# Performance work log

Measured on AMD Instinct MI355X. Metric: run time of the kernel, lower is better.

## Reference

```python
import jax, jax.numpy as jnp
import numpy as np

N_NODES = 100000
N_EDGES = 1600000
D = 64


def setup_inputs() -> dict:
    key = jax.random.key(0)
    ks = jax.random.split(key, 7)
    x = jax.random.normal(ks[0], (N_NODES, D), dtype=jnp.float32)
    row = jax.random.randint(ks[1], (N_EDGES,), 0, N_NODES, dtype=jnp.int64)
    col = jax.random.randint(ks[2], (N_EDGES,), 0, N_NODES, dtype=jnp.int64)
    batch = jnp.zeros((N_NODES,), dtype=jnp.int64)
    # positive normalizer (e.g. degree-based); keep away from zero
    adj_norm = jax.random.uniform(ks[3], (N_NODES, 1), dtype=jnp.float32, minval=0.5, maxval=1.5)
    root_W = jax.random.normal(ks[4], (D, D), dtype=jnp.float32) / jnp.sqrt(D)
    root_b = jax.random.normal(ks[5], (D,), dtype=jnp.float32) * 0.01
    rel_W = jax.random.normal(ks[6], (D, D), dtype=jnp.float32) / jnp.sqrt(D)
    return {"x": x, "row": row, "col": col, "batch": batch, "adj_norm": adj_norm,
            "root_W": root_W, "root_b": root_b, "rel_W": rel_W}


def reference(x, row, col, batch, adj_norm, root_W, root_b, rel_W):
    # gather source features per edge, scatter-sum into destination nodes
    agg = jax.ops.segment_sum(x[row], col, num_segments=x.shape[0])  # [N, D]
    agg = agg / adj_norm
    rel = agg @ rel_W.T                      # Linear(bias=False)
    root = x @ root_W.T + root_b             # Linear(bias=True)
    return jax.nn.relu(rel + root)
```

## Files before the change

### kernel.cpp

```cpp
#include <hip/hip_runtime.h>

#define N_NODES 100000
#define N_EDGES 1600000
#define D 64
#define ROWW 128
#define NPB 128
#define NBUCK ((N_NODES + NPB - 1) / NPB)
#define CHUNK 8192
#define NCHUNK ((N_EDGES + CHUNK - 1) / CHUNK)
#define APAD 136

typedef __attribute__((ext_vector_type(8))) short bf16x8;
typedef __attribute__((ext_vector_type(4))) float f32x4;

__device__ __forceinline__ unsigned short f2bf(float f) {
    unsigned bits = __float_as_uint(f);
    bits += 0x7FFF + ((bits >> 16) & 1);
    return (unsigned short)(bits >> 16);
}

__global__ __launch_bounds__(256) void stage_x(const float* __restrict__ x,
                                               unsigned short* __restrict__ ab, int n8) {
    int t = blockIdx.x * 256 + threadIdx.x;
    if (t >= n8) return;
    int nrow = t >> 3, g = t & 7;
    const float4* xf = (const float4*)(x + (size_t)nrow * D + g * 8);
    float4 a = xf[0], b = xf[1];
    unsigned short u[8];
    u[0] = f2bf(a.x); u[1] = f2bf(a.y); u[2] = f2bf(a.z); u[3] = f2bf(a.w);
    u[4] = f2bf(b.x); u[5] = f2bf(b.y); u[6] = f2bf(b.z); u[7] = f2bf(b.w);
    *reinterpret_cast<uint4*>(ab + (size_t)nrow * ROWW + 64 + g * 8) =
        *reinterpret_cast<const uint4*>(u);
}

__global__ __launch_bounds__(256) void stage_w(const float* __restrict__ rel_W,
                                               const float* __restrict__ root_W,
                                               unsigned short* __restrict__ Wb) {
    int t = blockIdx.x * 256 + threadIdx.x;
    if (t >= 1024) return;
    int j = t >> 4, g = t & 15;
    const float* src = (g < 8) ? (rel_W + j * 64 + g * 8) : (root_W + j * 64 + (g - 8) * 8);
    unsigned short u[8];
    #pragma unroll
    for (int i = 0; i < 8; ++i) u[i] = f2bf(src[i]);
    *reinterpret_cast<uint4*>(Wb + j * ROWW + g * 8) = *reinterpret_cast<const uint4*>(u);
}

__global__ __launch_bounds__(1024) void hist_kernel(const int* __restrict__ col,
                                                    int* __restrict__ bucketTotals) {
    __shared__ int h[NBUCK];
    for (int k = threadIdx.x; k < NBUCK; k += 1024) h[k] = 0;
    __syncthreads();
    int base = blockIdx.x * CHUNK;
    #pragma unroll
    for (int it = 0; it < CHUNK / 1024; ++it) {
        int e = base + it * 1024 + threadIdx.x;
        if (e < N_EDGES) atomicAdd(&h[col[e] >> 7], 1);
    }
    __syncthreads();
    for (int k = threadIdx.x; k < NBUCK; k += 1024)
        if (h[k]) atomicAdd(&bucketTotals[k], h[k]);
}

__global__ __launch_bounds__(1024) void scan_kernel(const int* __restrict__ totals,
                                                    int* __restrict__ base_,
                                                    int* __restrict__ cursor) {
    int tid = threadIdx.x;
    int v = (tid < NBUCK) ? totals[tid] : 0;
    int lane = tid & 63, wave = tid >> 6;
    int s = v;
    #pragma unroll
    for (int o = 1; o < 64; o <<= 1) {
        int t = __shfl_up(s, o, 64);
        if (lane >= o) s += t;
    }
    __shared__ int ws[16];
    if (lane == 63) ws[wave] = s;
    __syncthreads();
    if (wave == 0 && lane < 16) {
        int w = ws[lane];
        #pragma unroll
        for (int o = 1; o < 16; o <<= 1) {
            int t = __shfl_up(w, o, 64);
            if (lane >= o) w += t;
        }
        ws[lane] = w;
    }
    __syncthreads();
    int excl = s - v + (wave ? ws[wave - 1] : 0);
    if (tid < NBUCK) { base_[tid] = excl; cursor[tid] = excl; }
}

__global__ __launch_bounds__(1024) void partition_kernel(const int* __restrict__ row,
                                                         const int* __restrict__ col,
                                                         int* __restrict__ cursor,
                                                         int* __restrict__ edges) {
    __shared__ int cnt[NBUCK];
    __shared__ int runStart[NBUCK];
    __shared__ int rank[NBUCK];
    for (int k = threadIdx.x; k < NBUCK; k += 1024) { cnt[k] = 0; rank[k] = 0; }
    __syncthreads();
    int base = blockIdx.x * CHUNK;
    #pragma unroll
    for (int it = 0; it < CHUNK / 1024; ++it) {
        int e = base + it * 1024 + threadIdx.x;
        if (e < N_EDGES) atomicAdd(&cnt[col[e] >> 7], 1);
    }
    __syncthreads();
    for (int k = threadIdx.x; k < NBUCK; k += 1024) {
        int c = cnt[k];
        runStart[k] = c ? atomicAdd(&cursor[k], c) : 0;
    }
    __syncthreads();
    #pragma unroll
    for (int it = 0; it < CHUNK / 1024; ++it) {
        int e = base + it * 1024 + threadIdx.x;
        if (e < N_EDGES) {
            int d = col[e];
            int b = d >> 7;
            int r = atomicAdd(&rank[b], 1);
            edges[runStart[b] + r] = ((d & (NPB - 1)) << 17) | row[e];
        }
    }
}

__global__ __launch_bounds__(512) void sort_kernel(const int* __restrict__ edges,
                                                   const int* __restrict__ base_,
                                                   const int* __restrict__ totals,
                                                   int* __restrict__ edge_src,
                                                   int* __restrict__ off,
                                                   int* __restrict__ deg) {
    __shared__ int cnt[NPB];
    __shared__ int offL[NPB];
    __shared__ int cur[NPB];
    int tid = threadIdx.x;
    int b = blockIdx.x;
    int base = base_[b];
    int tot = totals[b];

    if (tid < NPB) cnt[tid] = 0;
    __syncthreads();
    for (int i = base + tid; i < base + tot; i += 512)
        atomicAdd(&cnt[edges[i] >> 17], 1);
    __syncthreads();

    if (tid < 64) {
        int v0 = cnt[2 * tid], v1 = cnt[2 * tid + 1];
        int s = v0 + v1;
        #pragma unroll
        for (int o = 1; o < 64; o <<= 1) {
            int t = __shfl_up(s, o, 64);
            if (tid >= o) s += t;
        }
        offL[2 * tid]     = s - v1 - v0;
        offL[2 * tid + 1] = s - v1;
        cur[2 * tid]      = s - v1 - v0;
        cur[2 * tid + 1]  = s - v1;
    }
    __syncthreads();

    for (int i = base + tid; i < base + tot; i += 512) {
        int p = edges[i];
        int l = p >> 17;
        int r = atomicAdd(&cur[l], 1);
        edge_src[base + r] = p & 0x1FFFF;
    }

    if (tid < NPB) {
        int gn = b * NPB + tid;
        if (gn < N_NODES) {
            off[gn] = base + offL[tid];
            deg[gn] = cnt[tid];
        }
    }
}

__global__ __launch_bounds__(256) void agg_kernel(unsigned short* __restrict__ ab,
                                                  const int* __restrict__ edge_src,
                                                  const int* __restrict__ off,
                                                  const int* __restrict__ deg,
                                                  const float* __restrict__ adj_norm) {
    int w = (blockIdx.x * 256 + threadIdx.x) >> 6;
    if (w >= N_NODES) return;
    int lane = threadIdx.x & 63;
    int q = lane >> 4, sub = lane & 15;
    int s = off[w], dg = deg[w];
    const unsigned short* __restrict__ xh = ab + 64 + sub * 4;

    float a0 = 0.f, a1 = 0.f, a2 = 0.f, a3 = 0.f;
    int base = 0;
    int idx = (lane < dg) ? edge_src[s + lane] : 0;

    while (true) {
        int lim = dg - base; if (lim > 64) lim = 64;
        int eb = 0;
        for (; eb + 16 <= lim; eb += 16) {
            int i0 = __shfl(idx, eb + q);
            int i1 = __shfl(idx, eb + q + 4);
            int i2 = __shfl(idx, eb + q + 8);
            int i3 = __shfl(idx, eb + q + 12);
            uint2 u0 = *reinterpret_cast<const uint2*>(xh + (size_t)i0 * ROWW);
            uint2 u1 = *reinterpret_cast<const uint2*>(xh + (size_t)i1 * ROWW);
            uint2 u2 = *reinterpret_cast<const uint2*>(xh + (size_t)i2 * ROWW);
            uint2 u3 = *reinterpret_cast<const uint2*>(xh + (size_t)i3 * ROWW);
            a0 += __uint_as_float(u0.x << 16) + __uint_as_float(u1.x << 16)
                + __uint_as_float(u2.x << 16) + __uint_as_float(u3.x << 16);
            a1 += __uint_as_float(u0.x & 0xffff0000u) + __uint_as_float(u1.x & 0xffff0000u)
                + __uint_as_float(u2.x & 0xffff0000u) + __uint_as_float(u3.x & 0xffff0000u);
            a2 += __uint_as_float(u0.y << 16) + __uint_as_float(u1.y << 16)
                + __uint_as_float(u2.y << 16) + __uint_as_float(u3.y << 16);
            a3 += __uint_as_float(u0.y & 0xffff0000u) + __uint_as_float(u1.y & 0xffff0000u)
                + __uint_as_float(u2.y & 0xffff0000u) + __uint_as_float(u3.y & 0xffff0000u);
        }
        if (eb < lim) {
            int nst = (lim - eb + 3) >> 2;
            for (int t = 0; t < nst; ++t) {
                int e = eb + q + t * 4;
                int ii = __shfl(idx, e & 63);
                uint2 u = *reinterpret_cast<const uint2*>(xh + (size_t)ii * ROWW);
                if (e < lim) {
                    a0 += __uint_as_float(u.x << 16);
                    a1 += __uint_as_float(u.x & 0xffff0000u);
                    a2 += __uint_as_float(u.y << 16);
                    a3 += __uint_as_float(u.y & 0xffff0000u);
                }
            }
        }
        base += 64;
        if (base >= dg) break;
        idx = (base + lane < dg) ? edge_src[s + base + lane] : 0;
    }

    a0 += __shfl_xor(a0, 16, 64); a0 += __shfl_xor(a0, 32, 64);
    a1 += __shfl_xor(a1, 16, 64); a1 += __shfl_xor(a1, 32, 64);
    a2 += __shfl_xor(a2, 16, 64); a2 += __shfl_xor(a2, 32, 64);
    a3 += __shfl_xor(a3, 16, 64); a3 += __shfl_xor(a3, 32, 64);

    if (q == 0) {
        float inv = 1.0f / adj_norm[w];
        uint2 p;
        p.x = (unsigned)f2bf(a0 * inv) | ((unsigned)f2bf(a1 * inv) << 16);
        p.y = (unsigned)f2bf(a2 * inv) | ((unsigned)f2bf(a3 * inv) << 16);
        *reinterpret_cast<uint2*>(ab + (size_t)w * ROWW + sub * 4) = p;
    }
}

__global__ __launch_bounds__(256) void fused_out_kernel(
    const unsigned short* __restrict__ ab, const unsigned short* __restrict__ Wb,
    const float* __restrict__ root_b, float* __restrict__ out)
{
    __shared__ unsigned short a_sh[64 * APAD];
    __shared__ unsigned short b_sh[64 * APAD];
    const int tid = threadIdx.x;
    const int n0 = blockIdx.x * 64;

    {
        int r = tid >> 2, seg = tid & 3;
        int gn = n0 + r;
        uint4 v0 = {0,0,0,0}, v1 = {0,0,0,0}, v2 = {0,0,0,0}, v3 = {0,0,0,0};
        if (gn < N_NODES) {
            const uint4* src = (const uint4*)(ab + (size_t)gn * ROWW + seg * 32);
            v0 = src[0]; v1 = src[1]; v2 = src[2]; v3 = src[3];
        }
        uint4* dst = (uint4*)(a_sh + r * APAD + seg * 32);
        dst[0] = v0; dst[1] = v1; dst[2] = v2; dst[3] = v3;
    }
    {
        int r = tid >> 2, seg = tid & 3;
        const uint4* src = (const uint4*)(Wb + r * ROWW + seg * 32);
        uint4* dst = (uint4*)(b_sh + r * APAD + seg * 32);
        dst[0] = src[0]; dst[1] = src[1]; dst[2] = src[2]; dst[3] = src[3];
    }
    __syncthreads();

    const int wv = tid >> 6, lane = tid & 63;
    const int quad = lane >> 4, l15 = lane & 15;

    bf16x8 afrag[4];
    const int abase = (wv * 16 + l15) * APAD + quad * 8;
    #pragma unroll
    for (int kk = 0; kk < 4; ++kk)
        afrag[kk] = *reinterpret_cast<const bf16x8*>(a_sh + abase + kk * 32);

    f32x4 acc[4] = {};
    #pragma unroll
    for (int t = 0; t < 4; ++t) {
        const int bbase = (t * 16 + l15) * APAD + quad * 8;
        #pragma unroll
        for (int kk = 0; kk < 4; ++kk) {
            bf16x8 bfrag = *reinterpret_cast<const bf16x8*>(b_sh + bbase + kk * 32);
            acc[t] = __builtin_amdgcn_mfma_f32_16x16x32_bf16(afrag[kk], bfrag, acc[t], 0, 0, 0);
        }
    }

    #pragma unroll
    for (int t = 0; t < 4; ++t) {
        int j = t * 16 + l15;
        float bias = root_b[j];
        #pragma unroll
        for (int r = 0; r < 4; ++r) {
            int node = n0 + wv * 16 + quad * 4 + r;
            if (node < N_NODES) {
                float v = acc[t][r] + bias;
                out[(size_t)node * D + j] = fmaxf(v, 0.0f);
            }
        }
    }
}

extern "C" void kernel_launch(void* const* d_in, const int* in_sizes, int n_in,
                              void* d_out, int out_size, void* d_ws, size_t ws_size,
                              hipStream_t stream)
{
    const float* x        = (const float*)d_in[0];
    const int*   row      = (const int*)d_in[1];
    const int*   col      = (const int*)d_in[2];
    const float* adj_norm = (const float*)d_in[4];
    const float* root_W   = (const float*)d_in[5];
    const float* root_b   = (const float*)d_in[6];
    const float* rel_W    = (const float*)d_in[7];
    float* out = (float*)d_out;

    char* ws = (char*)d_ws;
    unsigned short* ab = (unsigned short*)ws;  ws += (size_t)N_NODES * ROWW * 2;
    unsigned short* Wb = (unsigned short*)ws;  ws += 64 * ROWW * 2;
    int* bucketTot  = (int*)ws;  ws += ((size_t)NBUCK * 4 + 15) / 16 * 16;
    int* bucketBase = (int*)ws;  ws += ((size_t)NBUCK * 4 + 15) / 16 * 16;
    int* bucketCur  = (int*)ws;  ws += ((size_t)NBUCK * 4 + 15) / 16 * 16;
    int* off        = (int*)ws;  ws += (size_t)N_NODES * 4;
    int* deg        = (int*)ws;  ws += (size_t)N_NODES * 4;
    int* edges      = (int*)ws;  ws += (size_t)N_EDGES * 4;
    int* edge_src   = (int*)ws;

    hipMemsetAsync(bucketTot, 0, NBUCK * sizeof(int), stream);

    const int n8 = N_NODES * D / 8;
    stage_x<<<(n8 + 255) / 256, 256, 0, stream>>>(x, ab, n8);
    stage_w<<<4, 256, 0, stream>>>(rel_W, root_W, Wb);

    hist_kernel<<<NCHUNK, 1024, 0, stream>>>(col, bucketTot);
    scan_kernel<<<1, 1024, 0, stream>>>(bucketTot, bucketBase, bucketCur);
    partition_kernel<<<NCHUNK, 1024, 0, stream>>>(row, col, bucketCur, edges);
    sort_kernel<<<NBUCK, 512, 0, stream>>>(edges, bucketBase, bucketTot, edge_src, off, deg);

    const int aggThreads = N_NODES * 64;
    agg_kernel<<<(aggThreads + 255) / 256, 256, 0, stream>>>(ab, edge_src, off, deg, adj_norm);

    fused_out_kernel<<<(N_NODES + 63) / 64, 256, 0, stream>>>(ab, Wb, root_b, out);
}
```

Baseline: 189.0 us.

## Fuse preprocessing into one grid-synchronized kernel and merge aggregation with output GEMM

Collapses the staging, histogram, scan, partition and bucket-sort kernels into a single persistent kernel that separates phases with a software grid barrier. Aggregation and the output matmul are merged so each block aggregates 16 nodes into shared memory and immediately runs MFMA against the weights, removing the intermediate write and reread of aggregated rows. The staged bf16 x array shrinks to 64-wide rows, and edge indices are now loaded per lane instead of broadcast through shuffles. The grid barrier assumes all 196 blocks of 1024 threads are co-resident, which risks deadlock if they are not.

```diff
diff --git a/kernel.cpp b/kernel.cpp
--- a/kernel.cpp
+++ b/kernel.cpp
@@ -3,12 +3,13 @@
 #define N_NODES 100000
 #define N_EDGES 1600000
 #define D 64
-#define ROWW 128
+#define XROW 64
+#define WROW 128
 #define NPB 128
 #define NBUCK ((N_NODES + NPB - 1) / NPB)
 #define CHUNK 8192
 #define NCHUNK ((N_EDGES + CHUNK - 1) / CHUNK)
-#define APAD 136
+#define ASTRIDE 72
 
 typedef __attribute__((ext_vector_type(8))) short bf16x8;
 typedef __attribute__((ext_vector_type(4))) float f32x4;
@@ -19,216 +20,215 @@
     return (unsigned short)(bits >> 16);
 }
 
-__global__ __launch_bounds__(256) void stage_x(const float* __restrict__ x,
-                                               unsigned short* __restrict__ ab, int n8) {
-    int t = blockIdx.x * 256 + threadIdx.x;
-    if (t >= n8) return;
-    int nrow = t >> 3, g = t & 7;
-    const float4* xf = (const float4*)(x + (size_t)nrow * D + g * 8);
-    float4 a = xf[0], b = xf[1];
-    unsigned short u[8];
-    u[0] = f2bf(a.x); u[1] = f2bf(a.y); u[2] = f2bf(a.z); u[3] = f2bf(a.w);
-    u[4] = f2bf(b.x); u[5] = f2bf(b.y); u[6] = f2bf(b.z); u[7] = f2bf(b.w);
-    *reinterpret_cast<uint4*>(ab + (size_t)nrow * ROWW + 64 + g * 8) =
-        *reinterpret_cast<const uint4*>(u);
-}
-
-__global__ __launch_bounds__(256) void stage_w(const float* __restrict__ rel_W,
-                                               const float* __restrict__ root_W,
-                                               unsigned short* __restrict__ Wb) {
-    int t = blockIdx.x * 256 + threadIdx.x;
-    if (t >= 1024) return;
-    int j = t >> 4, g = t & 15;
-    const float* src = (g < 8) ? (rel_W + j * 64 + g * 8) : (root_W + j * 64 + (g - 8) * 8);
-    unsigned short u[8];
-    #pragma unroll
-    for (int i = 0; i < 8; ++i) u[i] = f2bf(src[i]);
-    *reinterpret_cast<uint4*>(Wb + j * ROWW + g * 8) = *reinterpret_cast<const uint4*>(u);
-}
-
-__global__ __launch_bounds__(1024) void hist_kernel(const int* __restrict__ col,
-                                                    int* __restrict__ bucketTotals) {
-    __shared__ int h[NBUCK];
-    for (int k = threadIdx.x; k < NBUCK; k += 1024) h[k] = 0;
-    __syncthreads();
-    int base = blockIdx.x * CHUNK;
-    #pragma unroll
-    for (int it = 0; it < CHUNK / 1024; ++it) {
-        int e = base + it * 1024 + threadIdx.x;
-        if (e < N_EDGES) atomicAdd(&h[col[e] >> 7], 1);
-    }
-    __syncthreads();
-    for (int k = threadIdx.x; k < NBUCK; k += 1024)
-        if (h[k]) atomicAdd(&bucketTotals[k], h[k]);
-}
-
-__global__ __launch_bounds__(1024) void scan_kernel(const int* __restrict__ totals,
-                                                    int* __restrict__ base_,
-                                                    int* __restrict__ cursor) {
-    int tid = threadIdx.x;
-    int v = (tid < NBUCK) ? totals[tid] : 0;
-    int lane = tid & 63, wave = tid >> 6;
-    int s = v;
-    #pragma unroll
-    for (int o = 1; o < 64; o <<= 1) {
-        int t = __shfl_up(s, o, 64);
-        if (lane >= o) s += t;
-    }
-    __shared__ int ws[16];
-    if (lane == 63) ws[wave] = s;
-    __syncthreads();
-    if (wave == 0 && lane < 16) {
-        int w = ws[lane];
-        #pragma unroll
-        for (int o = 1; o < 16; o <<= 1) {
-            int t = __shfl_up(w, o, 64);
-            if (lane >= o) w += t;
-        }
-        ws[lane] = w;
-    }
-    __syncthreads();
-    int excl = s - v + (wave ? ws[wave - 1] : 0);
-    if (tid < NBUCK) { base_[tid] = excl; cursor[tid] = excl; }
-}
-
-__global__ __launch_bounds__(1024) void partition_kernel(const int* __restrict__ row,
-                                                         const int* __restrict__ col,
-                                                         int* __restrict__ cursor,
-                                                         int* __restrict__ edges) {
-    __shared__ int cnt[NBUCK];
-    __shared__ int runStart[NBUCK];
-    __shared__ int rank[NBUCK];
-    for (int k = threadIdx.x; k < NBUCK; k += 1024) { cnt[k] = 0; rank[k] = 0; }
-    __syncthreads();
-    int base = blockIdx.x * CHUNK;
-    #pragma unroll
-    for (int it = 0; it < CHUNK / 1024; ++it) {
-        int e = base + it * 1024 + threadIdx.x;
-        if (e < N_EDGES) atomicAdd(&cnt[col[e] >> 7], 1);
-    }
-    __syncthreads();
-    for (int k = threadIdx.x; k < NBUCK; k += 1024) {
-        int c = cnt[k];
-        runStart[k] = c ? atomicAdd(&cursor[k], c) : 0;
-    }
-    __syncthreads();
-    #pragma unroll
-    for (int it = 0; it < CHUNK / 1024; ++it) {
-        int e = base + it * 1024 + threadIdx.x;
-        if (e < N_EDGES) {
-            int d = col[e];
-            int b = d >> 7;
-            int r = atomicAdd(&rank[b], 1);
-            edges[runStart[b] + r] = ((d & (NPB - 1)) << 17) | row[e];
-        }
-    }
-}
-
-__global__ __launch_bounds__(512) void sort_kernel(const int* __restrict__ edges,
-                                                   const int* __restrict__ base_,
-                                                   const int* __restrict__ totals,
-                                                   int* __restrict__ edge_src,
-                                                   int* __restrict__ off,
-                                                   int* __restrict__ deg) {
-    __shared__ int cnt[NPB];
-    __shared__ int offL[NPB];
-    __shared__ int cur[NPB];
-    int tid = threadIdx.x;
-    int b = blockIdx.x;
-    int base = base_[b];
-    int tot = totals[b];
-
-    if (tid < NPB) cnt[tid] = 0;
-    __syncthreads();
-    for (int i = base + tid; i < base + tot; i += 512)
-        atomicAdd(&cnt[edges[i] >> 17], 1);
-    __syncthreads();
-
-    if (tid < 64) {
-        int v0 = cnt[2 * tid], v1 = cnt[2 * tid + 1];
-        int s = v0 + v1;
+__device__ __forceinline__ void grid_bar(int* bar, int nblk) {
+    __syncthreads();
+    if (threadIdx.x == 0) {
+        int g = __hip_atomic_load(bar + 1, __ATOMIC_RELAXED, __HIP_MEMORY_SCOPE_AGENT);
+        __threadfence();
+        int a = __hip_atomic_fetch_add(bar, 1, __ATOMIC_ACQ_REL, __HIP_MEMORY_SCOPE_AGENT);
+        if (a == nblk - 1) {
+            __hip_atomic_store(bar, 0, __ATOMIC_RELAXED, __HIP_MEMORY_SCOPE_AGENT);
+            __hip_atomic_fetch_add(bar + 1, 1, __ATOMIC_ACQ_REL, __HIP_MEMORY_SCOPE_AGENT);
+        } else {
+            while (__hip_atomic_load(bar + 1, __ATOMIC_RELAXED, __HIP_MEMORY_SCOPE_AGENT) == g)
+                __builtin_amdgcn_s_sleep(8);
+        }
+        __threadfence();
+    }
+    __syncthreads();
+}
+
+__global__ __launch_bounds__(1024) void pre_kernel(
+    const float* __restrict__ x, const float* __restrict__ rel_W,
+    const float* __restrict__ root_W, const int* __restrict__ row,
+    const int* __restrict__ col,
+    unsigned short* __restrict__ ab, unsigned short* __restrict__ Wb,
+    int* __restrict__ bar, int* __restrict__ bucketTot,
+    int* __restrict__ bucketBase, int* __restrict__ bucketCur,
+    int* __restrict__ edges, int* __restrict__ edge_src,
+    int* __restrict__ off, int* __restrict__ deg)
+{
+    __shared__ int shm[3 * NBUCK];
+    const int tid  = threadIdx.x;
+    const int gtid = blockIdx.x * 1024 + tid;
+    const int nthr = NCHUNK * 1024;
+
+    for (int t = gtid; t < N_NODES * 8; t += nthr) {
+        int nrow = t >> 3, g = t & 7;
+        const float4* xf = (const float4*)(x + (size_t)nrow * D + g * 8);
+        float4 a = xf[0], b = xf[1];
+        unsigned short u[8];
+        u[0] = f2bf(a.x); u[1] = f2bf(a.y); u[2] = f2bf(a.z); u[3] = f2bf(a.w);
+        u[4] = f2bf(b.x); u[5] = f2bf(b.y); u[6] = f2bf(b.z); u[7] = f2bf(b.w);
+        *reinterpret_cast<uint4*>(ab + (size_t)nrow * XROW + g * 8) =
+            *reinterpret_cast<const uint4*>(u);
+    }
+    if (gtid < 1024) {
+        int j = gtid >> 4, g = gtid & 15;
+        const float* src = (g < 8) ? (rel_W + j * 64 + g * 8) : (root_W + j * 64 + (g - 8) * 8);
+        unsigned short u[8];
+        #pragma unroll
+        for (int i = 0; i < 8; ++i) u[i] = f2bf(src[i]);
+        *reinterpret_cast<uint4*>(Wb + j * WROW + g * 8) = *reinterpret_cast<const uint4*>(u);
+    }
+
+    for (int k = tid; k < NBUCK; k += 1024) shm[k] = 0;
+    __syncthreads();
+    {
+        int base = blockIdx.x * CHUNK;
+        #pragma unroll
+        for (int it = 0; it < CHUNK / 1024; ++it) {
+            int e = base + it * 1024 + tid;
+            if (e < N_EDGES) atomicAdd(&shm[col[e] >> 7], 1);
+        }
+    }
+    __syncthreads();
+    for (int k = tid; k < NBUCK; k += 1024)
+        if (shm[k]) atomicAdd(&bucketTot[k], shm[k]);
+
+    grid_bar(bar, gridDim.x);
+
+    if (blockIdx.x == 0) {
+        int v = (tid < NBUCK) ? bucketTot[tid] : 0;
+        int lane = tid & 63, wave = tid >> 6;
+        int s = v;
         #pragma unroll
         for (int o = 1; o < 64; o <<= 1) {
             int t = __shfl_up(s, o, 64);
-            if (tid >= o) s += t;
-        }
-        offL[2 * tid]     = s - v1 - v0;
-        offL[2 * tid + 1] = s - v1;
-        cur[2 * tid]      = s - v1 - v0;
-        cur[2 * tid + 1]  = s - v1;
-    }
-    __syncthreads();
-
-    for (int i = base + tid; i < base + tot; i += 512) {
-        int p = edges[i];
-        int l = p >> 17;
-        int r = atomicAdd(&cur[l], 1);
-        edge_src[base + r] = p & 0x1FFFF;
-    }
-
-    if (tid < NPB) {
-        int gn = b * NPB + tid;
-        if (gn < N_NODES) {
-            off[gn] = base + offL[tid];
-            deg[gn] = cnt[tid];
-        }
-    }
-}
-
-__global__ __launch_bounds__(256) void agg_kernel(unsigned short* __restrict__ ab,
-                                                  const int* __restrict__ edge_src,
-                                                  const int* __restrict__ off,
-                                                  const int* __restrict__ deg,
-                                                  const float* __restrict__ adj_norm) {
-    int w = (blockIdx.x * 256 + threadIdx.x) >> 6;
-    if (w >= N_NODES) return;
-    int lane = threadIdx.x & 63;
-    int q = lane >> 4, sub = lane & 15;
-    int s = off[w], dg = deg[w];
-    const unsigned short* __restrict__ xh = ab + 64 + sub * 4;
+            if (lane >= o) s += t;
+        }
+        if (lane == 63) shm[wave] = s;
+        __syncthreads();
+        if (wave == 0 && lane < 16) {
+            int w = shm[lane];
+            #pragma unroll
+            for (int o = 1; o < 16; o <<= 1) {
+                int t = __shfl_up(w, o, 64);
+                if (lane >= o) w += t;
+            }
+            shm[lane] = w;
+        }
+        __syncthreads();
+        int excl = s - v + (wave ? shm[wave - 1] : 0);
+        if (tid < NBUCK) { bucketBase[tid] = excl; bucketCur[tid] = excl; }
+    }
+
+    grid_bar(bar, gridDim.x);
+
+    {
+        int* cnt = shm; int* runStart = shm + NBUCK; int* rank = shm + 2 * NBUCK;
+        for (int k = tid; k < NBUCK; k += 1024) { cnt[k] = 0; rank[k] = 0; }
+        __syncthreads();
+        int base = blockIdx.x * CHUNK;
+        #pragma unroll
+        for (int it = 0; it < CHUNK / 1024; ++it) {
+            int e = base + it * 1024 + tid;
+            if (e < N_EDGES) atomicAdd(&cnt[col[e] >> 7], 1);
+        }
+        __syncthreads();
+        for (int k = tid; k < NBUCK; k += 1024) {
+            int c = cnt[k];
+            runStart[k] = c ? atomicAdd(&bucketCur[k], c) : 0;
+        }
+        __syncthreads();
+        #pragma unroll
+        for (int it = 0; it < CHUNK / 1024; ++it) {
+            int e = base + it * 1024 + tid;
+            if (e < N_EDGES) {
+                int d = col[e];
+                int b = d >> 7;
+                int r = atomicAdd(&rank[b], 1);
+                edges[runStart[b] + r] = ((d & (NPB - 1)) << 17) | row[e];
+            }
+        }
+    }
+
+    grid_bar(bar, gridDim.x);
+
+    {
+        int* cnt = shm; int* offL = shm + NPB; int* cur = shm + 2 * NPB;
+        for (int b = blockIdx.x; b < NBUCK; b += NCHUNK) {
+            int base = bucketBase[b];
+            int tot  = bucketTot[b];
+            if (tid < NPB) cnt[tid] = 0;
+            __syncthreads();
+            for (int i = base + tid; i < base + tot; i += 1024)
+                atomicAdd(&cnt[edges[i] >> 17], 1);
+            __syncthreads();
+            if (tid < 64) {
+                int v0 = cnt[2 * tid], v1 = cnt[2 * tid + 1];
+                int s = v0 + v1;
+                #pragma unroll
+                for (int o = 1; o < 64; o <<= 1) {
+                    int t = __shfl_up(s, o, 64);
+                    if (tid >= o) s += t;
+                }
+                offL[2 * tid]     = s - v1 - v0;
+                offL[2 * tid + 1] = s - v1;
+                cur[2 * tid]      = s - v1 - v0;
+                cur[2 * tid + 1]  = s - v1;
+            }
+            __syncthreads();
+            for (int i = base + tid; i < base + tot; i += 1024) {
+                int p = edges[i];
+                int l = p >> 17;
+                int r = atomicAdd(&cur[l], 1);
+                edge_src[base + r] = p & 0x1FFFF;
+            }
+            if (tid < NPB) {
+                int gn = b * NPB + tid;
+                if (gn < N_NODES) {
+                    off[gn] = base + offL[tid];
+                    deg[gn] = cnt[tid];
+                }
+            }
+            __syncthreads();
+        }
+    }
+}
+
+__global__ __launch_bounds__(1024, 8) void agg_out_kernel(
+    const unsigned short* __restrict__ ab, const int* __restrict__ edge_src,
+    const int* __restrict__ off, const int* __restrict__ deg,
+    const float* __restrict__ adj_norm, const unsigned short* __restrict__ Wb,
+    const float* __restrict__ root_b, float* __restrict__ out)
+{
+    __shared__ unsigned short a_sh[16 * ASTRIDE];
+    const int tid  = threadIdx.x;
+    const int wv   = tid >> 6;
+    const int lane = tid & 63;
+    const int q    = lane >> 4, sub = lane & 15;
+    const int n0   = blockIdx.x * 16;
+    const int n    = n0 + wv;
+
+    const int s  = off[n];
+    const int dg = deg[n];
+    const unsigned short* __restrict__ xh = ab + sub * 4;
 
     float a0 = 0.f, a1 = 0.f, a2 = 0.f, a3 = 0.f;
-    int base = 0;
-    int idx = (lane < dg) ? edge_src[s + lane] : 0;
-
-    while (true) {
-        int lim = dg - base; if (lim > 64) lim = 64;
-        int eb = 0;
-        for (; eb + 16 <= lim; eb += 16) {
-            int i0 = __shfl(idx, eb + q);
-            int i1 = __shfl(idx, eb + q + 4);
-            int i2 = __shfl(idx, eb + q + 8);
-            int i3 = __shfl(idx, eb + q + 12);
-            uint2 u0 = *reinterpret_cast<const uint2*>(xh + (size_t)i0 * ROWW);
-            uint2 u1 = *reinterpret_cast<const uint2*>(xh + (size_t)i1 * ROWW);
-            uint2 u2 = *reinterpret_cast<const uint2*>(xh + (size_t)i2 * ROWW);
-            uint2 u3 = *reinterpret_cast<const uint2*>(xh + (size_t)i3 * ROWW);
-            a0 += __uint_as_float(u0.x << 16) + __uint_as_float(u1.x << 16)
-                + __uint_as_float(u2.x << 16) + __uint_as_float(u3.x << 16);
-            a1 += __uint_as_float(u0.x & 0xffff0000u) + __uint_as_float(u1.x & 0xffff0000u)
-                + __uint_as_float(u2.x & 0xffff0000u) + __uint_as_float(u3.x & 0xffff0000u);
-            a2 += __uint_as_float(u0.y << 16) + __uint_as_float(u1.y << 16)
-                + __uint_as_float(u2.y << 16) + __uint_as_float(u3.y << 16);
-            a3 += __uint_as_float(u0.y & 0xffff0000u) + __uint_as_float(u1.y & 0xffff0000u)
-                + __uint_as_float(u2.y & 0xffff0000u) + __uint_as_float(u3.y & 0xffff0000u);
-        }
-        if (eb < lim) {
-            int nst = (lim - eb + 3) >> 2;
-            for (int t = 0; t < nst; ++t) {
-                int e = eb + q + t * 4;
-                int ii = __shfl(idx, e & 63);
-                uint2 u = *reinterpret_cast<const uint2*>(xh + (size_t)ii * ROWW);
-                if (e < lim) {
-                    a0 += __uint_as_float(u.x << 16);
-                    a1 += __uint_as_float(u.x & 0xffff0000u);
-                    a2 += __uint_as_float(u.y << 16);
-                    a3 += __uint_as_float(u.y & 0xffff0000u);
-                }
-            }
-        }
-        base += 64;
-        if (base >= dg) break;
-        idx = (base + lane < dg) ? edge_src[s + base + lane] : 0;
+    for (int e0 = 0; e0 < dg; e0 += 16) {
+        int e = e0 + q;
+        bool k0 = e < dg, k1 = e + 4 < dg, k2 = e + 8 < dg, k3 = e + 12 < dg;
+        int i0 = k0 ? edge_src[s + e]      : 0;
+        int i1 = k1 ? edge_src[s + e + 4]  : 0;
+        int i2 = k2 ? edge_src[s + e + 8]  : 0;
+        int i3 = k3 ? edge_src[s + e + 12] : 0;
+        uint2 u0 = *reinterpret_cast<const uint2*>(xh + (size_t)i0 * XROW);
+        uint2 u1 = *reinterpret_cast<const uint2*>(xh + (size_t)i1 * XROW);
+        uint2 u2 = *reinterpret_cast<const uint2*>(xh + (size_t)i2 * XROW);
+        uint2 u3 = *reinterpret_cast<const uint2*>(xh + (size_t)i3 * XROW);
+        if (!k0) { u0.x = 0u; u0.y = 0u; }
+        if (!k1) { u1.x = 0u; u1.y = 0u; }
+        if (!k2) { u2.x = 0u; u2.y = 0u; }
+        if (!k3) { u3.x = 0u; u3.y = 0u; }
+        a0 += __uint_as_float(u0.x << 16) + __uint_as_float(u1.x << 16)
+            + __uint_as_float(u2.x << 16) + __uint_as_float(u3.x << 16);
+        a1 += __uint_as_float(u0.x & 0xffff0000u) + __uint_as_float(u1.x & 0xffff0000u)
+            + __uint_as_float(u2.x & 0xffff0000u) + __uint_as_float(u3.x & 0xffff0000u);
+        a2 += __uint_as_float(u0.y << 16) + __uint_as_float(u1.y << 16)
+            + __uint_as_float(u2.y << 16) + __uint_as_float(u3.y << 16);
+        a3 += __uint_as_float(u0.y & 0xffff0000u) + __uint_as_float(u1.y & 0xffff0000u)
+            + __uint_as_float(u2.y & 0xffff0000u) + __uint_as_float(u3.y & 0xffff0000u);
     }
 
     a0 += __shfl_xor(a0, 16, 64); a0 += __shfl_xor(a0, 32, 64);
@@ -237,73 +237,34 @@
     a3 += __shfl_xor(a3, 16, 64); a3 += __shfl_xor(a3, 32, 64);
 
     if (q == 0) {
-        float inv = 1.0f / adj_norm[w];
+        float inv = 1.0f / adj_norm[n];
         uint2 p;
         p.x = (unsigned)f2bf(a0 * inv) | ((unsigned)f2bf(a1 * inv) << 16);
         p.y = (unsigned)f2bf(a2 * inv) | ((unsigned)f2bf(a3 * inv) << 16);
-        *reinterpret_cast<uint2*>(ab + (size_t)w * ROWW + sub * 4) = p;
-    }
-}
-
-__global__ __launch_bounds__(256) void fused_out_kernel(
-    const unsigned short* __restrict__ ab, const unsigned short* __restrict__ Wb,
-    const float* __restrict__ root_b, float* __restrict__ out)
-{
-    __shared__ unsigned short a_sh[64 * APAD];
-    __shared__ unsigned short b_sh[64 * APAD];
-    const int tid = threadIdx.x;
-    const int n0 = blockIdx.x * 64;
-
-    {
-        int r = tid >> 2, seg = tid & 3;
-        int gn = n0 + r;
-        uint4 v0 = {0,0,0,0}, v1 = {0,0,0,0}, v2 = {0,0,0,0}, v3 = {0,0,0,0};
-        if (gn < N_NODES) {
-            const uint4* src = (const uint4*)(ab + (size_t)gn * ROWW + seg * 32);
-            v0 = src[0]; v1 = src[1]; v2 = src[2]; v3 = src[3];
-        }
-        uint4* dst = (uint4*)(a_sh + r * APAD + seg * 32);
-        dst[0] = v0; dst[1] = v1; dst[2] = v2; dst[3] = v3;
-    }
-    {
-        int r = tid >> 2, seg = tid & 3;
-        const uint4* src = (const uint4*)(Wb + r * ROWW + seg * 32);
-        uint4* dst = (uint4*)(b_sh + r * APAD + seg * 32);
-        dst[0] = src[0]; dst[1] = src[1]; dst[2] = src[2]; dst[3] = src[3];
-    }
-    __syncthreads();
-
-    const int wv = tid >> 6, lane = tid & 63;
-    const int quad = lane >> 4, l15 = lane & 15;
-
-    bf16x8 afrag[4];
-    const int abase = (wv * 16 + l15) * APAD + quad * 8;
-    #pragma unroll
-    for (int kk = 0; kk < 4; ++kk)
-        afrag[kk] = *reinterpret_cast<const bf16x8*>(a_sh + abase + kk * 32);
-
-    f32x4 acc[4] = {};
-    #pragma unroll
-    for (int t = 0; t < 4; ++t) {
-        const int bbase = (t * 16 + l15) * APAD + quad * 8;
+        *reinterpret_cast<uint2*>(a_sh + wv * ASTRIDE + sub * 4) = p;
+    }
+    __syncthreads();
+
+    if (wv < 4) {
+        f32x4 c = {0.f, 0.f, 0.f, 0.f};
         #pragma unroll
         for (int kk = 0; kk < 4; ++kk) {
-            bf16x8 bfrag = *reinterpret_cast<const bf16x8*>(b_sh + bbase + kk * 32);
-            acc[t] = __builtin_amdgcn_mfma_f32_16x16x32_bf16(afrag[kk], bfrag, acc[t], 0, 0, 0);
-        }
-    }
-
-    #pragma unroll
-    for (int t = 0; t < 4; ++t) {
-        int j = t * 16 + l15;
+            bf16x8 af;
+            if (kk < 2)
+                af = *reinterpret_cast<const bf16x8*>(a_sh + sub * ASTRIDE + q * 8 + kk * 32);
+            else
+                af = *reinterpret_cast<const bf16x8*>(ab + (size_t)(n0 + sub) * XROW
+                                                      + q * 8 + (kk - 2) * 32);
+            bf16x8 bf = *reinterpret_cast<const bf16x8*>(Wb + (wv * 16 + sub) * WROW
+                                                         + q * 8 + kk * 32);
+            c = __builtin_amdgcn_mfma_f32_16x16x32_bf16(af, bf, c, 0, 0, 0);
+        }
+        int j = wv * 16 + sub;
         float bias = root_b[j];
         #pragma unroll
         for (int r = 0; r < 4; ++r) {
-            int node = n0 + wv * 16 + quad * 4 + r;
-            if (node < N_NODES) {
-                float v = acc[t][r] + bias;
-                out[(size_t)node * D + j] = fmaxf(v, 0.0f);
-            }
+            int node = n0 + q * 4 + r;
+            out[(size_t)node * D + j] = fmaxf(c[r] + bias, 0.0f);
         }
     }
 }
@@ -322,29 +283,23 @@
     float* out = (float*)d_out;
 
     char* ws = (char*)d_ws;
-    unsigned short* ab = (unsigned short*)ws;  ws += (size_t)N_NODES * ROWW * 2;
-    unsigned short* Wb = (unsigned short*)ws;  ws += 64 * ROWW * 2;
+    int* bar        = (int*)ws;  ws += 16;
     int* bucketTot  = (int*)ws;  ws += ((size_t)NBUCK * 4 + 15) / 16 * 16;
     int* bucketBase = (int*)ws;  ws += ((size_t)NBUCK * 4 + 15) / 16 * 16;
     int* bucketCur  = (int*)ws;  ws += ((size_t)NBUCK * 4 + 15) / 16 * 16;
+    unsigned short* ab = (unsigned short*)ws;  ws += (size_t)N_NODES * XROW * 2;
+    unsigned short* Wb = (unsigned short*)ws;  ws += 64 * WROW * 2;
     int* off        = (int*)ws;  ws += (size_t)N_NODES * 4;
     int* deg        = (int*)ws;  ws += (size_t)N_NODES * 4;
     int* edges      = (int*)ws;  ws += (size_t)N_EDGES * 4;
     int* edge_src   = (int*)ws;
 
-    hipMemsetAsync(bucketTot, 0, NBUCK * sizeof(int), stream);
-
-    const int n8 = N_NODES * D / 8;
-    stage_x<<<(n8 + 255) / 256, 256, 0, stream>>>(x, ab, n8);
-    stage_w<<<4, 256, 0, stream>>>(rel_W, root_W, Wb);
-
-    hist_kernel<<<NCHUNK, 1024, 0, stream>>>(col, bucketTot);
-    scan_kernel<<<1, 1024, 0, stream>>>(bucketTot, bucketBase, bucketCur);
-    partition_kernel<<<NCHUNK, 1024, 0, stream>>>(row, col, bucketCur, edges);
-    sort_kernel<<<NBUCK, 512, 0, stream>>>(edges, bucketBase, bucketTot, edge_src, off, deg);
-
-    const int aggThreads = N_NODES * 64;
-    agg_kernel<<<(aggThreads + 255) / 256, 256, 0, stream>>>(ab, edge_src, off, deg, adj_norm);
-
-    fused_out_kernel<<<(N_NODES + 63) / 64, 256, 0, stream>>>(ab, Wb, root_b, out);
-}
+    hipMemsetAsync(bar, 0, 16 + (size_t)NBUCK * 4, stream);
+
+    pre_kernel<<<NCHUNK, 1024, 0, stream>>>(x, rel_W, root_W, row, col, ab, Wb,
+                                            bar, bucketTot, bucketBase, bucketCur,
+                                            edges, edge_src, off, deg);
+
+    agg_out_kernel<<<N_NODES / 16, 1024, 0, stream>>>(ab, edge_src, off, deg,
+                                                      adj_norm, Wb, root_b, out);
+}
```

New measurement: 282.5 us. +49.5%, slower.
